# Kernel tuning notes

Hardware: AMD Instinct MI355X
Metric: run time of the kernel (lower is better)

The kernel has to match this reference:

```python
import jax, jax.numpy as jnp
import numpy as np

D_MODEL = 1024
N_HEADS = 16
D_K = D_MODEL // N_HEADS
LN_EPS = 1e-5


def setup_inputs() -> dict:
    key = jax.random.key(0)
    ks = jax.random.split(key, 12)
    B, S, D = 4, 2048, D_MODEL
    s = 1.0 / np.sqrt(D)
    return {
        "Q": jax.random.normal(ks[0], (B, S, D), jnp.float32),
        "K": jax.random.normal(ks[1], (B, S, D), jnp.float32),
        "V": jax.random.normal(ks[2], (B, S, D), jnp.float32),
        "W_q": jax.random.normal(ks[3], (D, D), jnp.float32) * s,
        "b_q": jnp.zeros((D,), jnp.float32),
        "W_k": jax.random.normal(ks[4], (D, D), jnp.float32) * s,
        "b_k": jnp.zeros((D,), jnp.float32),
        "W_v": jax.random.normal(ks[5], (D, D), jnp.float32) * s,
        "b_v": jnp.zeros((D,), jnp.float32),
        "W_o": jax.random.normal(ks[6], (D, D), jnp.float32) * s,
        "b_o": jnp.zeros((D,), jnp.float32),
        "ln_gamma": jnp.ones((D,), jnp.float32),
        "ln_beta": jnp.zeros((D,), jnp.float32),
    }


def _split_heads(x):  # (B,S,D) -> (B,H,S,Dk)
    B, S, _ = x.shape
    return x.reshape(B, S, N_HEADS, D_K).transpose(0, 2, 1, 3)


def reference(Q, K, V, W_q, b_q, W_k, b_k, W_v, b_v, W_o, b_o, ln_gamma, ln_beta):
    # Linear projections (torch Linear: x @ W^T + b)
    q = Q @ W_q.T + b_q  # (B,S,D) -- also the residual in this module
    k = K @ W_k.T + b_k
    v = V @ W_v.T + b_v
    qh, kh, vh = _split_heads(q), _split_heads(k), _split_heads(v)
    scale = 1.0 / jnp.sqrt(jnp.float32(D_K))
    scores = jnp.einsum("bhqd,bhkd->bhqk", qh, kh) * scale
    attn = jax.nn.softmax(scores, axis=-1)  # dropout = identity (eval)
    ctx = jnp.einsum("bhqk,bhkd->bhqd", attn, vh)
    B, H, S, Dk = ctx.shape
    ctx = ctx.transpose(0, 2, 1, 3).reshape(B, S, H * Dk)  # (B,S,D)
    out = ctx @ W_o.T + b_o
    # residual uses projected Q (module quirk), then LayerNorm
    x = out + q
    mu = jnp.mean(x, axis=-1, keepdims=True)
    var = jnp.mean((x - mu) ** 2, axis=-1, keepdims=True)
    return (x - mu) * jax.lax.rsqrt(var + LN_EPS) * ln_gamma + ln_beta
```

## Files before the change

### kernel.cpp

```cpp
#include <hip/hip_runtime.h>
#include <hip/hip_bf16.h>
#include <stdint.h>

#define D_MODEL 1024
#define NH 16
#define DKH 64
#define NBATCH 4
#define SEQ 2048
#define NROWS (NBATCH*SEQ)

typedef __bf16 bf16;
typedef __bf16 bf16x8 __attribute__((ext_vector_type(8)));
typedef __bf16 bf16x4 __attribute__((ext_vector_type(4)));
typedef float f32x4 __attribute__((ext_vector_type(4)));

static __device__ __forceinline__ f32x4 fzero4() {
  f32x4 z; z[0] = 0.f; z[1] = 0.f; z[2] = 0.f; z[3] = 0.f; return z;
}

static __device__ __forceinline__ float fast_exp2(float x) {
  return __builtin_amdgcn_exp2f(x);
}

static __device__ __forceinline__ void gload16(const bf16* g, bf16* lds) {
  __builtin_amdgcn_global_load_lds(
      (const __attribute__((address_space(1))) uint32_t*)(uintptr_t)g,
      (__attribute__((address_space(3))) uint32_t*)(uintptr_t)lds,
      16, 0, 0);
}

__global__ __launch_bounds__(256) void cvt3(const float* __restrict__ Q,
                                            const float* __restrict__ K,
                                            const float* __restrict__ V,
                                            bf16* __restrict__ out) {
  const int per4 = NROWS * D_MODEL / 4;
  const float* s = blockIdx.y == 0 ? Q : (blockIdx.y == 1 ? K : V);
  int i = blockIdx.x * 256 + threadIdx.x;
  float4 v = ((const float4*)s)[i];
  bf16x4 o;
  o[0] = (bf16)v.x; o[1] = (bf16)v.y; o[2] = (bf16)v.z; o[3] = (bf16)v.w;
  ((bf16x4*)out)[blockIdx.y * per4 + i] = o;
}

__global__ __launch_bounds__(256) void cvt_w4(const float* __restrict__ a,
                                              const float* __restrict__ b,
                                              const float* __restrict__ c,
                                              const float* __restrict__ d,
                                              bf16* __restrict__ out) {
  const float* srcs[4] = {a, b, c, d};
  const float* s = srcs[blockIdx.y];
  int i = blockIdx.x * 256 + threadIdx.x;
  float4 v = ((const float4*)s)[i];
  bf16x4 o;
  o[0] = (bf16)v.x; o[1] = (bf16)v.y; o[2] = (bf16)v.z; o[3] = (bf16)v.w;
  ((bf16x4*)out)[blockIdx.y * (D_MODEL * D_MODEL / 4) + i] = o;
}

#define STAGE_G(K0, BUF)                                                      \
  {                                                                           \
    _Pragma("unroll")                                                         \
    for (int i = 0; i < 4; i++) {                                             \
      int r = (w * 4 + i) * 8 + (l >> 3);                                     \
      int cb = ((l & 7) * 16) ^ ((r & 7) << 4);                               \
      gload16(A + (size_t)(rowA0 + r) * D_MODEL + (K0) + (cb >> 1),           \
              &As[BUF][(w * 4 + i) * 512]);                                   \
      gload16(B + (size_t)(colB0 + r) * D_MODEL + (K0) + (cb >> 1),           \
              &Bs[BUF][(w * 4 + i) * 512]);                                   \
    }                                                                         \
  }

__global__ __launch_bounds__(256) void gemm_qkv(const bf16* __restrict__ Ain,
                                                const bf16* __restrict__ Wall,
                                                const float* __restrict__ bq,
                                                const float* __restrict__ bk,
                                                const float* __restrict__ bv,
                                                bf16* __restrict__ qbf,
                                                bf16* __restrict__ kpb,
                                                bf16* __restrict__ vtb) {
  __shared__ __align__(16) bf16 As[2][128 * 64];
  __shared__ __align__(16) bf16 Bs[2][128 * 64];
  const int orig = blockIdx.x + ((blockIdx.y + (blockIdx.z << 6)) << 3);
  const int work = ((orig & 7) * 192) + (orig >> 3);
  const int bn = work & 7;
  const int bm = (work >> 3) & 63;
  const int z = work >> 9;

  const bf16* A = Ain + (size_t)z * NROWS * D_MODEL;
  const bf16* B = Wall + (size_t)z * D_MODEL * D_MODEL;
  const float* bias = z == 0 ? bq : (z == 1 ? bk : bv);
  const int N = D_MODEL;

  const int t = threadIdx.x, w = t >> 6, l = t & 63;
  const int wm = w >> 1, wn = w & 1;
  const int lr = l & 15, g = l >> 4;
  const int rowA0 = bm * 128, colB0 = bn * 128;

  f32x4 acc[4][4];
#pragma unroll
  for (int m = 0; m < 4; m++)
#pragma unroll
    for (int n = 0; n < 4; n++) acc[m][n] = fzero4();

  STAGE_G(0, 0);
  STAGE_G(64, 1);
  int cur = 0;
  for (int kt = 0; kt < 16; ++kt) {
    if (kt < 15) asm volatile("s_waitcnt vmcnt(8)" ::: "memory");
    else         asm volatile("s_waitcnt vmcnt(0)" ::: "memory");
    __builtin_amdgcn_s_barrier();
    asm volatile("" ::: "memory");
#pragma unroll
    for (int kk = 0; kk < 2; kk++) {
      bf16x8 av[4], bv4[4];
#pragma unroll
      for (int m = 0; m < 4; m++) {
        int row = wm * 64 + m * 16 + lr;
        int off = row * 128 + ((kk * 64 + g * 16) ^ ((row & 7) << 4));
        av[m] = *(const bf16x8*)((const char*)As[cur] + off);
      }
#pragma unroll
      for (int n = 0; n < 4; n++) {
        int row = wn * 64 + n * 16 + lr;
        int off = row * 128 + ((kk * 64 + g * 16) ^ ((row & 7) << 4));
        bv4[n] = *(const bf16x8*)((const char*)Bs[cur] + off);
      }
#pragma unroll
      for (int m = 0; m < 4; m++)
#pragma unroll
        for (int n = 0; n < 4; n++)
          acc[m][n] = __builtin_amdgcn_mfma_f32_16x16x32_bf16(av[m], bv4[n], acc[m][n], 0, 0, 0);
    }
    asm volatile("s_waitcnt lgkmcnt(0)" ::: "memory");
    __builtin_amdgcn_s_barrier();
    if (kt < 14) STAGE_G((kt + 2) * 64, cur);
    cur ^= 1;
  }

  if (z == 2) {
#pragma unroll
    for (int n = 0; n < 4; n++) {
      int col = colB0 + wn * 64 + n * 16 + lr;
      float bc = bias[col];
      int hh = col >> 6, dh = col & 63;
#pragma unroll
      for (int m = 0; m < 4; m++) {
        int row = rowA0 + wm * 64 + m * 16 + g * 4;
        int bb = row >> 11;
        int ss = row & 2047;
        int pos = (ss & ~31) + g * 8 + (m & 1) * 4;
        bf16x4 o;
#pragma unroll
        for (int j = 0; j < 4; j++) o[j] = (bf16)(acc[m][n][j] + bc);
        *(bf16x4*)(vtb + (((size_t)(bb * NH + hh)) * DKH + dh) * SEQ + pos) = o;
      }
    }
  } else {
    bf16* Cb = z == 0 ? qbf : kpb;
    const float bscale = z == 0 ? 0.180336880111f : 1.0f;
#pragma unroll
    for (int n = 0; n < 4; n++) {
      int col = colB0 + wn * 64 + n * 16 + lr;
      float bc = bias[col];
#pragma unroll
      for (int m = 0; m < 4; m++) {
#pragma unroll
        for (int j = 0; j < 4; j++) {
          int row = rowA0 + wm * 64 + m * 16 + g * 4 + j;
          Cb[(size_t)row * N + col] = (bf16)((acc[m][n][j] + bc) * bscale);
        }
      }
    }
  }
}

__global__ __launch_bounds__(256) void gemm_o(const bf16* __restrict__ A,
                                              const bf16* __restrict__ B,
                                              const float* __restrict__ bias,
                                              float* __restrict__ Cf) {
  __shared__ __align__(16) bf16 As[2][128 * 64];
  __shared__ __align__(16) bf16 Bs[2][128 * 64];
  const int orig = blockIdx.x + (blockIdx.y << 3);
  const int work = ((orig & 7) * 64) + (orig >> 3);
  const int bn = work & 7, bm = work >> 3;
  const int t = threadIdx.x, w = t >> 6, l = t & 63;
  const int wm = w >> 1, wn = w & 1;
  const int lr = l & 15, g = l >> 4;
  const int rowA0 = bm * 128, colB0 = bn * 128;
  const int N = D_MODEL;

  f32x4 acc[4][4];
#pragma unroll
  for (int m = 0; m < 4; m++)
#pragma unroll
    for (int n = 0; n < 4; n++) acc[m][n] = fzero4();

  STAGE_G(0, 0);
  STAGE_G(64, 1);
  int cur = 0;
  for (int kt = 0; kt < 16; ++kt) {
    if (kt < 15) asm volatile("s_waitcnt vmcnt(8)" ::: "memory");
    else         asm volatile("s_waitcnt vmcnt(0)" ::: "memory");
    __builtin_amdgcn_s_barrier();
    asm volatile("" ::: "memory");
#pragma unroll
    for (int kk = 0; kk < 2; kk++) {
      bf16x8 av[4], bv4[4];
#pragma unroll
      for (int m = 0; m < 4; m++) {
        int row = wm * 64 + m * 16 + lr;
        int off = row * 128 + ((kk * 64 + g * 16) ^ ((row & 7) << 4));
        av[m] = *(const bf16x8*)((const char*)As[cur] + off);
      }
#pragma unroll
      for (int n = 0; n < 4; n++) {
        int row = wn * 64 + n * 16 + lr;
        int off = row * 128 + ((kk * 64 + g * 16) ^ ((row & 7) << 4));
        bv4[n] = *(const bf16x8*)((const char*)Bs[cur] + off);
      }
#pragma unroll
      for (int m = 0; m < 4; m++)
#pragma unroll
        for (int n = 0; n < 4; n++)
          acc[m][n] = __builtin_amdgcn_mfma_f32_16x16x32_bf16(av[m], bv4[n], acc[m][n], 0, 0, 0);
    }
    asm volatile("s_waitcnt lgkmcnt(0)" ::: "memory");
    __builtin_amdgcn_s_barrier();
    if (kt < 14) STAGE_G((kt + 2) * 64, cur);
    cur ^= 1;
  }

#pragma unroll
  for (int n = 0; n < 4; n++) {
    int col = colB0 + wn * 64 + n * 16 + lr;
    float bc = bias[col];
#pragma unroll
    for (int m = 0; m < 4; m++) {
#pragma unroll
      for (int j = 0; j < 4; j++) {
        int row = rowA0 + wm * 64 + m * 16 + g * 4 + j;
        Cf[(size_t)row * N + col] = acc[m][n][j] + bc;
      }
    }
  }
}

__global__ __launch_bounds__(256, 4) void attn_fwd(const bf16* __restrict__ Qp,
                                                   const bf16* __restrict__ Kp,
                                                   const bf16* __restrict__ Vt,
                                                   bf16* __restrict__ Ctx) {
  __shared__ __align__(16) bf16 Ks[2][64 * 64];
  __shared__ __align__(16) bf16 Vs[2][64 * 64];
  const int bid0 = blockIdx.x;
  const int bid = ((bid0 & 7) << 7) | (bid0 >> 3);
  const int qt = bid & 15;
  const int h = (bid >> 4) & 15;
  const int b = bid >> 8;
  const int w = threadIdx.x >> 6, l = threadIdx.x & 63;
  const int lr = l & 15, g = l >> 4;
  const int q0 = qt * 128 + w * 32;

  const size_t qkBase = ((size_t)b * SEQ) * D_MODEL + h * DKH;
  const size_t vtBase = ((size_t)(b * NH + h)) * DKH * SEQ;
  const bf16* Kg = Kp + qkBase;
  const bf16* Vg = Vt + vtBase;

  const int sr = w * 8 + (l >> 3);
  const int scb = (l & 7) * 16;

  bf16x8 qf[2][2];
#pragma unroll
  for (int f = 0; f < 2; f++)
#pragma unroll
    for (int kk = 0; kk < 2; kk++)
      qf[f][kk] = *(const bf16x8*)(Qp + qkBase + (size_t)(q0 + f * 16 + lr) * D_MODEL + kk * 32 + g * 8);

  bf16x8 vone;
#pragma unroll
  for (int j = 0; j < 8; j++) vone[j] = (bf16)1.0f;

  f32x4 ctx[2][5];
#pragma unroll
  for (int f = 0; f < 2; f++)
#pragma unroll
    for (int n = 0; n < 5; n++) ctx[f][n] = fzero4();

#define STAGE(T, BUF)                                                         \
  {                                                                           \
    const int _s0 = (T) * 64;                                                 \
    _Pragma("unroll")                                                         \
    for (int i = 0; i < 2; i++) {                                             \
      int r = i * 32 + sr;                                                    \
      int cb = scb ^ ((r & 7) << 4);                                          \
      gload16(Kg + (size_t)(_s0 + r) * D_MODEL + (cb >> 1),                   \
              &Ks[BUF][i * 2048 + w * 512]);                                  \
      gload16(Vg + (size_t)r * SEQ + _s0 + (cb >> 1),                         \
              &Vs[BUF][i * 2048 + w * 512]);                                  \
    }                                                                         \
  }

  STAGE(0, 0);
  int cur = 0;
  for (int t = 0; t < SEQ / 64; ++t) {
    if (t + 1 < SEQ / 64) {
      STAGE(t + 1, cur ^ 1);
      asm volatile("s_waitcnt vmcnt(4)" ::: "memory");
    } else {
      asm volatile("s_waitcnt vmcnt(0)" ::: "memory");
    }
    __builtin_amdgcn_s_barrier();
    asm volatile("" ::: "memory");

#pragma unroll
    for (int ss = 0; ss < 2; ++ss) {
      bf16x8 ka[2][2];
#pragma unroll
      for (int hf = 0; hf < 2; hf++) {
        int row = ss * 32 + hf * 16 + lr;
#pragma unroll
        for (int kk = 0; kk < 2; kk++) {
          int off = row * 128 + ((kk * 64 + g * 16) ^ ((row & 7) << 4));
          ka[hf][kk] = *(const bf16x8*)((const char*)Ks[cur] + off);
        }
      }
      bf16x8 vb[4];
#pragma unroll
      for (int n = 0; n < 4; n++) {
        int row = n * 16 + lr;
        int off = row * 128 + ((ss * 64 + g * 16) ^ ((row & 7) << 4));
        vb[n] = *(const bf16x8*)((const char*)Vs[cur] + off);
      }

#pragma unroll
      for (int f = 0; f < 2; f++) {
        f32x4 sc[2];
        __builtin_amdgcn_s_setprio(1);
#pragma unroll
        for (int hf = 0; hf < 2; hf++) {
          f32x4 tt = fzero4();
          tt = __builtin_amdgcn_mfma_f32_16x16x32_bf16(ka[hf][0], qf[f][0], tt, 0, 0, 0);
          tt = __builtin_amdgcn_mfma_f32_16x16x32_bf16(ka[hf][1], qf[f][1], tt, 0, 0, 0);
          sc[hf] = tt;
        }
        __builtin_amdgcn_s_setprio(0);
        float p[8];
#pragma unroll
        for (int hf = 0; hf < 2; hf++)
#pragma unroll
          for (int j = 0; j < 4; j++)
            p[hf * 4 + j] = fast_exp2(sc[hf][j]);
        bf16x8 pa;
#pragma unroll
        for (int j = 0; j < 8; j++) pa[j] = (bf16)p[j];
        __builtin_amdgcn_s_setprio(1);
#pragma unroll
        for (int n = 0; n < 4; n++)
          ctx[f][n] = __builtin_amdgcn_mfma_f32_16x16x32_bf16(pa, vb[n], ctx[f][n], 0, 0, 0);
        ctx[f][4] = __builtin_amdgcn_mfma_f32_16x16x32_bf16(pa, vone, ctx[f][4], 0, 0, 0);
        __builtin_amdgcn_s_setprio(0);
      }
    }
    asm volatile("" ::: "memory");
    __builtin_amdgcn_s_barrier();
    cur ^= 1;
  }
#undef STAGE

#pragma unroll
  for (int f = 0; f < 2; f++) {
#pragma unroll
    for (int j = 0; j < 4; j++) {
      float lj = 1.0f / ctx[f][4][j];
      int s = q0 + f * 16 + g * 4 + j;
      size_t base = ((size_t)b * SEQ + s) * D_MODEL + h * DKH;
#pragma unroll
      for (int n = 0; n < 4; n++)
        Ctx[base + n * 16 + lr] = (bf16)(ctx[f][n][j] * lj);
    }
  }
}

__global__ __launch_bounds__(256) void ln_res(const float* __restrict__ O,
                                              const bf16* __restrict__ Rb,
                                              const float* __restrict__ gam,
                                              const float* __restrict__ bet,
                                              float* __restrict__ out) {
  const int row = blockIdx.x, t = threadIdx.x;
  const size_t idx = (size_t)row * 256 + t;
  const float4 o = ((const float4*)O)[idx];
  const bf16x4 rb = ((const bf16x4*)Rb)[idx];
  const float rs = 5.545177444479562f;
  float x0 = o.x + (float)rb[0] * rs, x1 = o.y + (float)rb[1] * rs;
  float x2 = o.z + (float)rb[2] * rs, x3 = o.w + (float)rb[3] * rs;
  float s = x0 + x1 + x2 + x3;
  float q = x0 * x0 + x1 * x1 + x2 * x2 + x3 * x3;
#pragma unroll
  for (int off = 32; off >= 1; off >>= 1) {
    s += __shfl_xor(s, off);
    q += __shfl_xor(q, off);
  }
  __shared__ float red[8];
  const int wid = t >> 6;
  if ((t & 63) == 0) { red[wid] = s; red[4 + wid] = q; }
  __syncthreads();
  s = red[0] + red[1] + red[2] + red[3];
  q = red[4] + red[5] + red[6] + red[7];
  const float mu = s * (1.f / 1024.f);
  const float rinv = rsqrtf(q * (1.f / 1024.f) - mu * mu + 1e-5f);
  const float4 g4 = ((const float4*)gam)[t];
  const float4 b4 = ((const float4*)bet)[t];
  float4 y;
  y.x = (x0 - mu) * rinv * g4.x + b4.x;
  y.y = (x1 - mu) * rinv * g4.y + b4.y;
  y.z = (x2 - mu) * rinv * g4.z + b4.z;
  y.w = (x3 - mu) * rinv * g4.w + b4.w;
  ((float4*)out)[idx] = y;
}

extern "C" void kernel_launch(void* const* d_in, const int* in_sizes, int n_in,
                              void* d_out, int out_size, void* d_ws, size_t ws_size,
                              hipStream_t stream) {
  const float* Q   = (const float*)d_in[0];
  const float* Kx  = (const float*)d_in[1];
  const float* V   = (const float*)d_in[2];
  const float* Wq  = (const float*)d_in[3];
  const float* bq  = (const float*)d_in[4];
  const float* Wk  = (const float*)d_in[5];
  const float* bk  = (const float*)d_in[6];
  const float* Wv  = (const float*)d_in[7];
  const float* bv  = (const float*)d_in[8];
  const float* Wo  = (const float*)d_in[9];
  const float* bo  = (const float*)d_in[10];
  const float* gam = (const float*)d_in[11];
  const float* bet = (const float*)d_in[12];
  float* out = (float*)d_out;

  char* ws = (char*)d_ws;
  const size_t MB = 1ull << 20;
  bf16* abf  = (bf16*)(ws);
  bf16* wall = (bf16*)(ws + 48 * MB);
  bf16* qbf  = (bf16*)(ws + 56 * MB);
  bf16* kpb  = (bf16*)(ws + 72 * MB);
  bf16* vtb  = (bf16*)(ws + 88 * MB);
  bf16* ctx  = (bf16*)(ws);
  float* attnout = (float*)(ws + 16 * MB);

  const int nW4 = D_MODEL * D_MODEL / 4;
  dim3 cb(256);

  cvt3<<<dim3(NROWS * D_MODEL / 4 / 256, 3), cb, 0, stream>>>(Q, Kx, V, abf);
  cvt_w4<<<dim3(nW4 / 256, 4), cb, 0, stream>>>(Wq, Wk, Wv, Wo, wall);

  gemm_qkv<<<dim3(8, 64, 3), cb, 0, stream>>>(abf, wall, bq, bk, bv, qbf, kpb, vtb);

  attn_fwd<<<NBATCH * NH * 16, cb, 0, stream>>>(qbf, kpb, vtb, ctx);

  gemm_o<<<dim3(8, 64), cb, 0, stream>>>(ctx, wall + 3ull * D_MODEL * D_MODEL, bo, attnout);
  ln_res<<<NROWS, cb, 0, stream>>>(attnout, qbf, gam, bet, out);
}
```

Measured before the change: 196.7 us.

## Fuse fp32-to-bf16 activation conversion into QKV GEMM A-tile loading

Removes the separate cvt3 kernel, which converted Q/K/V to bf16 in global memory. The QKV GEMM now loads the fp32 activations into registers, converts them, and writes swizzled bf16 into LDS, while the weights still use async global_load_lds. This avoids writing and re-reading 48MB of bf16 activations and one launch. The cost is that each GEMM tile reads fp32 A, which doubles A-side traffic across the 8 column blocks that share it. The load pipeline also becomes register-staged, with a full vmcnt(0) wait each iteration, which may expose latency.

New measurement: 194.6 us. No clear change (-1.1%).

```diff
diff --git a/kernel.cpp b/kernel.cpp
--- a/kernel.cpp
+++ b/kernel.cpp
@@ -27,19 +27,6 @@
       (const __attribute__((address_space(1))) uint32_t*)(uintptr_t)g,
       (__attribute__((address_space(3))) uint32_t*)(uintptr_t)lds,
       16, 0, 0);
-}
-
-__global__ __launch_bounds__(256) void cvt3(const float* __restrict__ Q,
-                                            const float* __restrict__ K,
-                                            const float* __restrict__ V,
-                                            bf16* __restrict__ out) {
-  const int per4 = NROWS * D_MODEL / 4;
-  const float* s = blockIdx.y == 0 ? Q : (blockIdx.y == 1 ? K : V);
-  int i = blockIdx.x * 256 + threadIdx.x;
-  float4 v = ((const float4*)s)[i];
-  bf16x4 o;
-  o[0] = (bf16)v.x; o[1] = (bf16)v.y; o[2] = (bf16)v.z; o[3] = (bf16)v.w;
-  ((bf16x4*)out)[blockIdx.y * per4 + i] = o;
 }
 
 __global__ __launch_bounds__(256) void cvt_w4(const float* __restrict__ a,
@@ -56,20 +43,9 @@
   ((bf16x4*)out)[blockIdx.y * (D_MODEL * D_MODEL / 4) + i] = o;
 }
 
-#define STAGE_G(K0, BUF)                                                      \
-  {                                                                           \
-    _Pragma("unroll")                                                         \
-    for (int i = 0; i < 4; i++) {                                             \
-      int r = (w * 4 + i) * 8 + (l >> 3);                                     \
-      int cb = ((l & 7) * 16) ^ ((r & 7) << 4);                               \
-      gload16(A + (size_t)(rowA0 + r) * D_MODEL + (K0) + (cb >> 1),           \
-              &As[BUF][(w * 4 + i) * 512]);                                   \
-      gload16(B + (size_t)(colB0 + r) * D_MODEL + (K0) + (cb >> 1),           \
-              &Bs[BUF][(w * 4 + i) * 512]);                                   \
-    }                                                                         \
-  }
-
-__global__ __launch_bounds__(256) void gemm_qkv(const bf16* __restrict__ Ain,
+__global__ __launch_bounds__(256) void gemm_qkv(const float* __restrict__ Qin,
+                                                const float* __restrict__ Kin,
+                                                const float* __restrict__ Vin,
                                                 const bf16* __restrict__ Wall,
                                                 const float* __restrict__ bq,
                                                 const float* __restrict__ bk,
@@ -85,7 +61,7 @@
   const int bm = (work >> 3) & 63;
   const int z = work >> 9;
 
-  const bf16* A = Ain + (size_t)z * NROWS * D_MODEL;
+  const float* A = z == 0 ? Qin : (z == 1 ? Kin : Vin);
   const bf16* B = Wall + (size_t)z * D_MODEL * D_MODEL;
   const float* bias = z == 0 ? bq : (z == 1 ? bk : bv);
   const int N = D_MODEL;
@@ -95,20 +71,59 @@
   const int lr = l & 15, g = l >> 4;
   const int rowA0 = bm * 128, colB0 = bn * 128;
 
+  const int c8 = l & 7;
+  const int rbase = l >> 3;
+
+  f32x4 a0[4], a1[4];
+
+#define LOADA(K0)                                                             \
+  {                                                                           \
+    _Pragma("unroll")                                                         \
+    for (int i = 0; i < 4; i++) {                                             \
+      int r = (w * 4 + i) * 8 + rbase;                                        \
+      const float* p = A + (size_t)(rowA0 + r) * D_MODEL + (K0) + c8 * 8;     \
+      a0[i] = *(const f32x4*)p;                                               \
+      a1[i] = *(const f32x4*)(p + 4);                                         \
+    }                                                                         \
+  }
+#define WRITEA(BUF)                                                           \
+  {                                                                           \
+    _Pragma("unroll")                                                         \
+    for (int i = 0; i < 4; i++) {                                             \
+      int r = (w * 4 + i) * 8 + rbase;                                        \
+      bf16x8 o;                                                               \
+      _Pragma("unroll")                                                       \
+      for (int j = 0; j < 4; j++) { o[j] = (bf16)a0[i][j]; o[4 + j] = (bf16)a1[i][j]; } \
+      *(bf16x8*)((char*)As[BUF] + r * 128 + ((c8 * 16) ^ ((r & 7) << 4))) = o; \
+    }                                                                         \
+  }
+#define STAGEB(K0, BUF)                                                       \
+  {                                                                           \
+    _Pragma("unroll")                                                         \
+    for (int i = 0; i < 4; i++) {                                             \
+      int r = (w * 4 + i) * 8 + rbase;                                        \
+      int cb = (c8 * 16) ^ ((r & 7) << 4);                                    \
+      gload16(B + (size_t)(colB0 + r) * D_MODEL + (K0) + (cb >> 1),           \
+              &Bs[BUF][(w * 4 + i) * 512]);                                   \
+    }                                                                         \
+  }
+
   f32x4 acc[4][4];
 #pragma unroll
   for (int m = 0; m < 4; m++)
 #pragma unroll
     for (int n = 0; n < 4; n++) acc[m][n] = fzero4();
 
-  STAGE_G(0, 0);
-  STAGE_G(64, 1);
+  LOADA(0); STAGEB(0, 0);
+  asm volatile("s_waitcnt vmcnt(0)" ::: "memory");
+  WRITEA(0);
+  asm volatile("s_waitcnt lgkmcnt(0)" ::: "memory");
+  __builtin_amdgcn_s_barrier();
+  asm volatile("" ::: "memory");
+  LOADA(64); STAGEB(64, 1);
+
   int cur = 0;
   for (int kt = 0; kt < 16; ++kt) {
-    if (kt < 15) asm volatile("s_waitcnt vmcnt(8)" ::: "memory");
-    else         asm volatile("s_waitcnt vmcnt(0)" ::: "memory");
-    __builtin_amdgcn_s_barrier();
-    asm volatile("" ::: "memory");
 #pragma unroll
     for (int kk = 0; kk < 2; kk++) {
       bf16x8 av[4], bv4[4];
@@ -130,11 +145,19 @@
         for (int n = 0; n < 4; n++)
           acc[m][n] = __builtin_amdgcn_mfma_f32_16x16x32_bf16(av[m], bv4[n], acc[m][n], 0, 0, 0);
     }
+    if (kt < 15) {
+      asm volatile("s_waitcnt vmcnt(0)" ::: "memory");
+      WRITEA(cur ^ 1);
+    }
     asm volatile("s_waitcnt lgkmcnt(0)" ::: "memory");
     __builtin_amdgcn_s_barrier();
-    if (kt < 14) STAGE_G((kt + 2) * 64, cur);
+    asm volatile("" ::: "memory");
+    if (kt < 14) { LOADA((kt + 2) * 64); STAGEB((kt + 2) * 64, cur); }
     cur ^= 1;
   }
+#undef LOADA
+#undef WRITEA
+#undef STAGEB
 
   if (z == 2) {
 #pragma unroll
@@ -172,6 +195,19 @@
     }
   }
 }
+
+#define STAGE_G(K0, BUF)                                                      \
+  {                                                                           \
+    _Pragma("unroll")                                                         \
+    for (int i = 0; i < 4; i++) {                                             \
+      int r = (w * 4 + i) * 8 + (l >> 3);                                     \
+      int cb = ((l & 7) * 16) ^ ((r & 7) << 4);                               \
+      gload16(A + (size_t)(rowA0 + r) * D_MODEL + (K0) + (cb >> 1),           \
+              &As[BUF][(w * 4 + i) * 512]);                                   \
+      gload16(B + (size_t)(colB0 + r) * D_MODEL + (K0) + (cb >> 1),           \
+              &Bs[BUF][(w * 4 + i) * 512]);                                   \
+    }                                                                         \
+  }
 
 __global__ __launch_bounds__(256) void gemm_o(const bf16* __restrict__ A,
                                               const bf16* __restrict__ B,
@@ -436,21 +472,19 @@
 
   char* ws = (char*)d_ws;
   const size_t MB = 1ull << 20;
-  bf16* abf  = (bf16*)(ws);
-  bf16* wall = (bf16*)(ws + 48 * MB);
-  bf16* qbf  = (bf16*)(ws + 56 * MB);
-  bf16* kpb  = (bf16*)(ws + 72 * MB);
-  bf16* vtb  = (bf16*)(ws + 88 * MB);
-  bf16* ctx  = (bf16*)(ws);
-  float* attnout = (float*)(ws + 16 * MB);
+  bf16* wall = (bf16*)(ws);
+  bf16* qbf  = (bf16*)(ws + 8 * MB);
+  bf16* kpb  = (bf16*)(ws + 24 * MB);
+  bf16* vtb  = (bf16*)(ws + 40 * MB);
+  bf16* ctx  = (bf16*)(ws + 56 * MB);
+  float* attnout = (float*)(ws + 72 * MB);
 
   const int nW4 = D_MODEL * D_MODEL / 4;
   dim3 cb(256);
 
-  cvt3<<<dim3(NROWS * D_MODEL / 4 / 256, 3), cb, 0, stream>>>(Q, Kx, V, abf);
   cvt_w4<<<dim3(nW4 / 256, 4), cb, 0, stream>>>(Wq, Wk, Wv, Wo, wall);
 
-  gemm_qkv<<<dim3(8, 64, 3), cb, 0, stream>>>(abf, wall, bq, bk, bv, qbf, kpb, vtb);
+  gemm_qkv<<<dim3(8, 64, 3), cb, 0, stream>>>(Q, Kx, V, wall, bq, bk, bv, qbf, kpb, vtb);
 
   attn_fwd<<<NBATCH * NH * 16, cb, 0, stream>>>(qbf, kpb, vtb, ctx);
 
```
